# Performance work log

Hardware: AMD Instinct MI355X
Metric: run time of the kernel (lower is better)

Reference implementation:

```python
import jax, jax.numpy as jnp
import numpy as np

FACTOR = 5


def setup_inputs() -> dict:
    key = jax.random.key(0)
    k1, k2, k3, k4 = jax.random.split(key, 4)
    B, L, H, D = 4, 2048, 8, 64
    sample_k = min(FACTOR * int(np.ceil(np.log(L))), L)  # 40
    return {
        "query": jax.random.normal(k1, (B, L, H, D), dtype=jnp.float32),
        "key": jax.random.normal(k2, (B, L, H, D), dtype=jnp.float32),
        "value": jax.random.normal(k3, (B, L, H, D), dtype=jnp.float32),
        "index_sample": jax.random.randint(k4, (L, sample_k), 0, L, dtype=jnp.int32),
    }


def reference(query, key, value, index_sample):
    # query/key/value: (B, L, H, D); mask_flag=True, output_attention=False
    B, L_Q, H, D = query.shape
    L_K = key.shape[1]
    q = jnp.swapaxes(query, 1, 2)  # (B,H,L_Q,D)
    k = jnp.swapaxes(key, 1, 2)    # (B,H,L_K,D)
    v = jnp.swapaxes(value, 1, 2)  # (B,H,L_K,D)

    U_part = min(FACTOR * int(np.ceil(np.log(L_K))), L_K)  # sample_k
    u = min(FACTOR * int(np.ceil(np.log(L_Q))), L_Q)       # n_top

    # --- _prob_QK: sampled QK scores, sparsity measure M, top-u queries ---
    # K_sample: gather sample_k keys per query position -> (B,H,L_Q,sample_k,D)
    K_sample = k[:, :, index_sample, :]
    Q_K_sample = jnp.einsum("bhid,bhisd->bhis", q, K_sample)  # (B,H,L_Q,sample_k)
    M = Q_K_sample.max(axis=-1) - Q_K_sample.sum(axis=-1) / L_K  # (B,H,L_Q)
    _, M_top = jax.lax.top_k(M, u)  # (B,H,u) indices of selected queries

    Q_reduce = jnp.take_along_axis(q, M_top[..., None], axis=2)  # (B,H,u,D)
    scores = jnp.einsum("bhud,bhkd->bhuk", Q_reduce, k)          # (B,H,u,L_K)

    scale = 1.0 / jnp.sqrt(jnp.float32(D))
    scores = scores * scale

    # --- initial context: causal cumsum of V (mask_flag=True) ---
    context = jnp.cumsum(v, axis=2)  # (B,H,L_Q,D)

    # --- update context: causal ProbMask on selected rows, softmax, scatter ---
    # mask[b,h,t,kk] = kk > M_top[b,h,t]
    mask = jnp.arange(L_K)[None, None, None, :] > M_top[..., None]
    scores = jnp.where(mask, -jnp.inf, scores)
    attn = jax.nn.softmax(scores, axis=-1)
    ctx_upd = jnp.einsum("bhuk,bhkd->bhud", attn, v)  # (B,H,u,D)

    b_idx = jnp.arange(context.shape[0])[:, None, None]
    h_idx = jnp.arange(context.shape[1])[None, :, None]
    context = context.at[b_idx, h_idx, M_top].set(ctx_upd)

    return jnp.swapaxes(context, 1, 2)  # (B, L_Q, H, D)
```

## Files before the change

### kernel.cpp

```cpp
#include <hip/hip_runtime.h>
#include <hip/hip_bf16.h>
#include <math.h>

constexpr int B = 4;
constexpr int L = 2048;
constexpr int H = 8;
constexpr int D = 64;
constexpr int S = 40;
constexpr int U = 40;
constexpr int C = 32;
constexpr int CHUNK = L / C;
constexpr int NSEG = 16;
constexpr int SEG  = L / NSEG;
constexpr int PAH  = 688;

__global__ void fused_Mpart(const float* __restrict__ q,
                            const float* __restrict__ k,
                            const float* __restrict__ v,
                            const int*   __restrict__ samp,
                            float* __restrict__ M,
                            float* __restrict__ part) {
    __shared__ float pa[H * PAH];
    int tid = threadIdx.x;

    if (blockIdx.x < 256) {
        int idx = blockIdx.x * 256 + tid;
        int b   = idx >> 14;
        int rem = idx & 16383;
        int c   = rem >> 9;
        int hd  = rem & 511;
        const float* base = v + ((size_t)(b * L + c * CHUNK) * H * D) + hd;
        float s = 0.f;
        for (int i = 0; i < CHUNK; i++) s += base[(size_t)i * (H * D)];
        int h = hd >> 6, d = hd & 63;
        part[((size_t)(b * H + h) * C + c) * D + d] = s;
        return;
    }

    int blk = blockIdx.x - 256;
    int xcd = blk & 7;
    int b   = xcd >> 1;
    int l   = ((blk >> 3) << 1) | (xcd & 1);
    int h      = tid >> 5;
    int lane32 = tid & 31;
    int g  = lane32 >> 4;
    int d4 = lane32 & 15;

    const float4 qv = *(const float4*)(q + ((size_t)(b * L + l) * H + h) * D + d4 * 4);
    const int* srow = samp + l * S;
    float* pah = pa + h * PAH;

#pragma unroll 10
    for (int sb = 0; sb < S; sb += 2) {
        int i0 = srow[sb];
        int i1 = srow[sb + 1];
        int idx = g ? i1 : i0;
        int s = sb + g;
        float4 kv = *(const float4*)(k + ((size_t)(b * L + idx) * H + h) * D + d4 * 4);
        pah[s * 17 + d4] = qv.x * kv.x + qv.y * kv.y + qv.z * kv.z + qv.w * kv.w;
    }
    __syncthreads();

    int s1 = lane32;
    float t0 = 0.f, t1 = 0.f, t2 = 0.f, t3 = 0.f;
#pragma unroll
    for (int i = 0; i < 16; i += 4) {
        t0 += pah[s1 * 17 + i];
        t1 += pah[s1 * 17 + i + 1];
        t2 += pah[s1 * 17 + i + 2];
        t3 += pah[s1 * 17 + i + 3];
    }
    float dot1 = (t0 + t1) + (t2 + t3);
    float mv = dot1, sv = dot1;
    if (lane32 < S - 32) {
        int s2 = 32 + lane32;
        float u0 = 0.f, u1 = 0.f, u2 = 0.f, u3 = 0.f;
#pragma unroll
        for (int i = 0; i < 16; i += 4) {
            u0 += pah[s2 * 17 + i];
            u1 += pah[s2 * 17 + i + 1];
            u2 += pah[s2 * 17 + i + 2];
            u3 += pah[s2 * 17 + i + 3];
        }
        float dot2 = (u0 + u1) + (u2 + u3);
        mv = fmaxf(mv, dot2);
        sv += dot2;
    }
#pragma unroll
    for (int off = 1; off <= 16; off <<= 1) {
        mv = fmaxf(mv, __shfl_xor(mv, off));
        sv += __shfl_xor(sv, off);
    }
    if (lane32 == 0) M[(size_t)(b * H + h) * L + l] = mv - sv * (1.0f / (float)L);
}

__global__ void fused_topk_cumsum(const float* __restrict__ M,
                                  const float* __restrict__ v,
                                  const float* __restrict__ part,
                                  int* __restrict__ Mtop,
                                  float* __restrict__ out) {
    int tid = threadIdx.x;

    if (blockIdx.x >= 32) {
        int idx = (blockIdx.x - 32) * 64 + tid;
        int b   = idx >> 14;
        int rem = idx & 16383;
        int c   = rem >> 9;
        int hd  = rem & 511;
        int h = hd >> 6, d = hd & 63;

        float run = 0.f;
        for (int cc = 0; cc < c; cc++)
            run += part[((size_t)(b * H + h) * C + cc) * D + d];

        const float* base  = v   + ((size_t)(b * L + c * CHUNK) * H * D) + hd;
        float*       obase = out + ((size_t)(b * L + c * CHUNK) * H * D) + hd;
        for (int i = 0; i < CHUNK; i++) {
            run += base[(size_t)i * (H * D)];
            obase[(size_t)i * (H * D)] = run;
        }
        return;
    }

    int bh   = blockIdx.x;
    int base = tid * 32;
    const float* row = M + (size_t)bh * L;

    unsigned int vals[32];
#pragma unroll
    for (int r4 = 0; r4 < 8; r4++) {
        float4 f = *(const float4*)(row + base + r4 * 4);
        const float ff[4] = {f.x, f.y, f.z, f.w};
#pragma unroll
        for (int j = 0; j < 4; j++) {
            unsigned int i = __float_as_uint(ff[j]);
            vals[r4 * 4 + j] = (i & 0x80000000u) ? ~i : (i | 0x80000000u);
        }
    }

    unsigned long long k1 = 0ull, k2 = 0ull;
#pragma unroll
    for (int r = 0; r < 32; r++) {
        unsigned long long kk =
            ((unsigned long long)vals[r] << 32) | (unsigned int)~(base + r);
        if (kk > k1) { k2 = k1; k1 = kk; }
        else if (kk > k2) { k2 = kk; }
    }

    for (int it = 0; it < U; it += 2) {
        unsigned long long a1 = k1, a2 = k2;
#pragma unroll
        for (int off = 1; off < 64; off <<= 1) {
            unsigned long long o1 = __shfl_xor(a1, off);
            unsigned long long o2 = __shfl_xor(a2, off);
            unsigned long long hi = a1 > o1 ? a1 : o1;
            unsigned long long lo = a1 > o1 ? o1 : a1;
            unsigned long long ss = a2 > o2 ? a2 : o2;
            a1 = hi;
            a2 = lo > ss ? lo : ss;
        }
        int i1 = (int)~(unsigned int)a1;
        int i2 = (int)~(unsigned int)a2;
        if (tid == 0) {
            Mtop[bh * U + it]     = i1;
            Mtop[bh * U + it + 1] = i2;
        }
        bool own1 = (i1 >> 5) == tid;
        bool own2 = (i2 >> 5) == tid;
        if (own1 | own2) {
            int r1 = own1 ? (i1 & 31) : 32;
            int r2 = own2 ? (i2 & 31) : 32;
#pragma unroll
            for (int r = 0; r < 32; r++)
                if (r == r1 || r == r2) vals[r] = 0u;
            k1 = 0ull; k2 = 0ull;
#pragma unroll
            for (int r = 0; r < 32; r++) {
                unsigned long long kk =
                    ((unsigned long long)vals[r] << 32) | (unsigned int)~(base + r);
                if (kk > k1) { k2 = k1; k1 = kk; }
                else if (kk > k2) { k2 = kk; }
            }
        }
    }
}

__global__ __launch_bounds__(256, 2)
void attn_batched(const float* __restrict__ q,
                  const float* __restrict__ k,
                  const float* __restrict__ v,
                  const int*   __restrict__ Mtop,
                  float* __restrict__ ml,
                  float* __restrict__ pacc) {
    int blk = blockIdx.x;
    int xcd = blk & 7;
    int b   = xcd >> 1;
    int r   = ((blk >> 3) << 1) | (xcd & 1);
    int h   = r >> 4;
    int seg = r & 15;
    int bh  = b * H + h;
    int j0  = seg * SEG;
    int tid = threadIdx.x;

    __shared__ float Qs[U * D];
    __shared__ float KV[SEG * D];
    __shared__ float Sc[U * SEG];
    __shared__ float red[U * 4];
    __shared__ float mrow[U];
    __shared__ int   qis[U];

    if (tid < U) qis[tid] = Mtop[bh * U + tid];
    __syncthreads();

    for (int i = tid; i < U * 16; i += 256) {
        int u = i >> 4, d4 = i & 15;
        *(float4*)&Qs[u * D + d4 * 4] =
            *(const float4*)(q + ((size_t)(b * L + qis[u]) * H + h) * D + d4 * 4);
    }
    for (int i = tid; i < SEG * 16; i += 256) {
        int rr = i >> 4, d4 = i & 15;
        float4 kv = *(const float4*)(k + ((size_t)(b * L + j0 + rr) * H + h) * D + d4 * 4);
        *(float4*)&KV[rr * D + (d4 ^ (rr & 15)) * 4] = kv;
    }
    __syncthreads();

    int ug = tid >> 5;
    int jg = tid & 31;
    int jlow = jg & 15;
    float acc[5][4];
#pragma unroll
    for (int uu = 0; uu < 5; uu++)
#pragma unroll
        for (int jj = 0; jj < 4; jj++) acc[uu][jj] = 0.f;

#pragma unroll
    for (int kk4 = 0; kk4 < 16; kk4++) {
        float4 kf[4];
        int slot = kk4 ^ jlow;
#pragma unroll
        for (int jj = 0; jj < 4; jj++)
            kf[jj] = *(const float4*)&KV[(jg + 32 * jj) * D + slot * 4];
#pragma unroll
        for (int uu = 0; uu < 5; uu++) {
            float4 qf = *(const float4*)&Qs[(ug * 5 + uu) * D + kk4 * 4];
#pragma unroll
            for (int jj = 0; jj < 4; jj++) {
                acc[uu][jj] += qf.x * kf[jj].x + qf.y * kf[jj].y
                             + qf.z * kf[jj].z + qf.w * kf[jj].w;
            }
        }
    }
#pragma unroll
    for (int uu = 0; uu < 5; uu++) {
        int u = ug * 5 + uu;
        int um = u & 15;
#pragma unroll
        for (int jj = 0; jj < 4; jj++) {
            int j = jg + 32 * jj;
            Sc[u * SEG + 4 * ((j >> 2) ^ um) + (j & 3)] = acc[uu][jj] * 0.125f;
        }
    }
    __syncthreads();

    for (int i = tid; i < SEG * 16; i += 256) {
        int rr = i >> 4, d4 = i & 15;
        float4 vv = *(const float4*)(v + ((size_t)(b * L + j0 + rr) * H + h) * D + d4 * 4);
        *(float4*)&KV[rr * D + (d4 ^ (rr & 15)) * 4] = vv;
    }

    int su = tid >> 2, sq = tid & 3;
    int nkc = 0;
    if (tid < U * 4) {
        int nk = qis[su] + 1 - j0;
        nkc = nk < 0 ? 0 : (nk > SEG ? SEG : nk);
        int um = su & 15;
        float mvx = -INFINITY;
        for (int t = 0; t < 32; t++) {
            int i = sq + 4 * t;
            if (i < nkc) mvx = fmaxf(mvx, Sc[su * SEG + 4 * ((i >> 2) ^ um) + (i & 3)]);
        }
        red[su * 4 + sq] = mvx;
    }
    __syncthreads();
    if (tid < U) {
        float m = fmaxf(fmaxf(red[tid * 4], red[tid * 4 + 1]),
                        fmaxf(red[tid * 4 + 2], red[tid * 4 + 3]));
        mrow[tid] = m;
    }
    __syncthreads();
    if (tid < U * 4) {
        float m = mrow[su];
        int um = su & 15;
        float ls = 0.f;
        for (int t = 0; t < 32; t++) {
            int i = sq + 4 * t;
            int addr = su * SEG + 4 * ((i >> 2) ^ um) + (i & 3);
            float e = 0.f;
            if (i < nkc) e = __expf(Sc[addr] - m);
            Sc[addr] = e;
            ls += e;
        }
        red[su * 4 + sq] = ls;
    }
    __syncthreads();
    if (tid < U) {
        float ls = (red[tid * 4] + red[tid * 4 + 1]) + (red[tid * 4 + 2] + red[tid * 4 + 3]);
        size_t mli = 2 * ((size_t)(bh * U + tid) * NSEG + seg);
        ml[mli]     = mrow[tid];
        ml[mli + 1] = ls;
    }

    int vg = jg;
    float a2[5][2];
#pragma unroll
    for (int uu = 0; uu < 5; uu++) { a2[uu][0] = 0.f; a2[uu][1] = 0.f; }

    for (int j4 = 0; j4 < 32; j4++) {
        float4 pf[5];
#pragma unroll
        for (int uu = 0; uu < 5; uu++) {
            int u = ug * 5 + uu;
            pf[uu] = *(const float4*)&Sc[u * SEG + 4 * (j4 ^ (u & 15))];
        }
#pragma unroll
        for (int jj = 0; jj < 4; jj++) {
            int j = j4 * 4 + jj;
            int fo = 4 * ((vg >> 1) ^ (j & 15)) + ((2 * vg) & 3);
            float2 vv = *(const float2*)&KV[j * D + fo];
#pragma unroll
            for (int uu = 0; uu < 5; uu++) {
                float p = ((const float*)&pf[uu])[jj];
                a2[uu][0] += p * vv.x;
                a2[uu][1] += p * vv.y;
            }
        }
    }
#pragma unroll
    for (int uu = 0; uu < 5; uu++) {
        int u = ug * 5 + uu;
        float2 w2 = make_float2(a2[uu][0], a2[uu][1]);
        *(float2*)&pacc[((size_t)(bh * U + u) * NSEG + seg) * D + 2 * vg] = w2;
    }
}

__global__ void attn_combine(const int* __restrict__ Mtop,
                             const float* __restrict__ ml,
                             const float* __restrict__ pacc,
                             float* __restrict__ out) {
    int blk = blockIdx.x;
    int u  = blk % U;
    int bh = blk / U;
    int h  = bh % H;
    int b  = bh / H;
    int d  = threadIdx.x;
    int qi = Mtop[bh * U + u];

    size_t r0 = (size_t)blk * NSEG;
    float m = -INFINITY;
#pragma unroll
    for (int s = 0; s < NSEG; s++) m = fmaxf(m, ml[2 * (r0 + s)]);

    float lt = 0.f, acc = 0.f;
#pragma unroll
    for (int s = 0; s < NSEG; s++) {
        float ms = ml[2 * (r0 + s)];
        float w  = __expf(ms - m);
        lt  += ml[2 * (r0 + s) + 1] * w;
        acc += pacc[(r0 + s) * D + d] * w;
    }
    out[((size_t)(b * L + qi) * H + h) * D + d] = acc / lt;
}

extern "C" void kernel_launch(void* const* d_in, const int* in_sizes, int n_in,
                              void* d_out, int out_size, void* d_ws, size_t ws_size,
                              hipStream_t stream) {
    const float* q    = (const float*)d_in[0];
    const float* k    = (const float*)d_in[1];
    const float* v    = (const float*)d_in[2];
    const int*   samp = (const int*)d_in[3];
    float* out = (float*)d_out;

    float* M    = (float*)d_ws;
    int*   Mtop = (int*)(M + (size_t)B * H * L);
    float* part = (float*)(Mtop + (size_t)B * H * U);
    float* ml   = part + (size_t)B * H * C * D;
    float* pacc = ml + (size_t)B * H * U * NSEG * 2;

    fused_Mpart<<<256 + B * L, 256, 0, stream>>>(q, k, v, samp, M, part);
    fused_topk_cumsum<<<32 + 1024, 64, 0, stream>>>(M, v, part, Mtop, out);
    attn_batched<<<B * H * NSEG, 256, 0, stream>>>(q, k, v, Mtop, ml, pacc);
    attn_combine<<<B * H * U, 64, 0, stream>>>(Mtop, ml, pacc, out);
}
```

Measured before the change: 184.2 us.

## Fuse softmax into score registers with shuffles; vectorize PV; widen cumsum blocks

```diff
diff --git a/kernel.cpp b/kernel.cpp
--- a/kernel.cpp
+++ b/kernel.cpp
@@ -102,7 +102,7 @@
     int tid = threadIdx.x;
 
     if (blockIdx.x >= 32) {
-        int idx = (blockIdx.x - 32) * 64 + tid;
+        int idx = (blockIdx.x - 32) * 256 + tid;
         int b   = idx >> 14;
         int rem = idx & 16383;
         int c   = rem >> 9;
@@ -122,6 +122,7 @@
         return;
     }
 
+    if (tid >= 64) return;
     int bh   = blockIdx.x;
     int base = tid * 32;
     const float* row = M + (size_t)bh * L;
@@ -205,8 +206,6 @@
     __shared__ float Qs[U * D];
     __shared__ float KV[SEG * D];
     __shared__ float Sc[U * SEG];
-    __shared__ float red[U * 4];
-    __shared__ float mrow[U];
     __shared__ int   qis[U];
 
     if (tid < U) qis[tid] = Mtop[bh * U + tid];
@@ -250,14 +249,39 @@
             }
         }
     }
+
 #pragma unroll
     for (int uu = 0; uu < 5; uu++) {
-        int u = ug * 5 + uu;
+        int u  = ug * 5 + uu;
         int um = u & 15;
+        int nk = qis[u] + 1 - j0;
+        nk = nk < 0 ? 0 : (nk > SEG ? SEG : nk);
+        float sc4[4];
+        float mv = -INFINITY;
 #pragma unroll
         for (int jj = 0; jj < 4; jj++) {
             int j = jg + 32 * jj;
-            Sc[u * SEG + 4 * ((j >> 2) ^ um) + (j & 3)] = acc[uu][jj] * 0.125f;
+            sc4[jj] = acc[uu][jj] * 0.125f;
+            if (j < nk) mv = fmaxf(mv, sc4[jj]);
+        }
+#pragma unroll
+        for (int off = 1; off <= 16; off <<= 1)
+            mv = fmaxf(mv, __shfl_xor(mv, off));
+        float ls = 0.f;
+#pragma unroll
+        for (int jj = 0; jj < 4; jj++) {
+            int j = jg + 32 * jj;
+            float e = (j < nk) ? __expf(sc4[jj] - mv) : 0.f;
+            Sc[u * SEG + 4 * ((j >> 2) ^ um) + (j & 3)] = e;
+            ls += e;
+        }
+#pragma unroll
+        for (int off = 1; off <= 16; off <<= 1)
+            ls += __shfl_xor(ls, off);
+        if (jg == 0) {
+            size_t mli = 2 * ((size_t)(bh * U + u) * NSEG + seg);
+            ml[mli]     = mv;
+            ml[mli + 1] = ls;
         }
     }
     __syncthreads();
@@ -267,55 +291,18 @@
         float4 vv = *(const float4*)(v + ((size_t)(b * L + j0 + rr) * H + h) * D + d4 * 4);
         *(float4*)&KV[rr * D + (d4 ^ (rr & 15)) * 4] = vv;
     }
-
-    int su = tid >> 2, sq = tid & 3;
-    int nkc = 0;
-    if (tid < U * 4) {
-        int nk = qis[su] + 1 - j0;
-        nkc = nk < 0 ? 0 : (nk > SEG ? SEG : nk);
-        int um = su & 15;
-        float mvx = -INFINITY;
-        for (int t = 0; t < 32; t++) {
-            int i = sq + 4 * t;
-            if (i < nkc) mvx = fmaxf(mvx, Sc[su * SEG + 4 * ((i >> 2) ^ um) + (i & 3)]);
-        }
-        red[su * 4 + sq] = mvx;
-    }
-    __syncthreads();
-    if (tid < U) {
-        float m = fmaxf(fmaxf(red[tid * 4], red[tid * 4 + 1]),
-                        fmaxf(red[tid * 4 + 2], red[tid * 4 + 3]));
-        mrow[tid] = m;
-    }
-    __syncthreads();
-    if (tid < U * 4) {
-        float m = mrow[su];
-        int um = su & 15;
-        float ls = 0.f;
-        for (int t = 0; t < 32; t++) {
-            int i = sq + 4 * t;
-            int addr = su * SEG + 4 * ((i >> 2) ^ um) + (i & 3);
-            float e = 0.f;
-            if (i < nkc) e = __expf(Sc[addr] - m);
-            Sc[addr] = e;
-            ls += e;
-        }
-        red[su * 4 + sq] = ls;
-    }
-    __syncthreads();
-    if (tid < U) {
-        float ls = (red[tid * 4] + red[tid * 4 + 1]) + (red[tid * 4 + 2] + red[tid * 4 + 3]);
-        size_t mli = 2 * ((size_t)(bh * U + tid) * NSEG + seg);
-        ml[mli]     = mrow[tid];
-        ml[mli + 1] = ls;
-    }
-
-    int vg = jg;
-    float a2[5][2];
-#pragma unroll
-    for (int uu = 0; uu < 5; uu++) { a2[uu][0] = 0.f; a2[uu][1] = 0.f; }
-
-    for (int j4 = 0; j4 < 32; j4++) {
+    __syncthreads();
+
+    int r5 = tid & 31;
+    int dg = r5 >> 1;
+    int jh = r5 & 1;
+    float4 a4[5];
+#pragma unroll
+    for (int uu = 0; uu < 5; uu++) a4[uu] = make_float4(0.f, 0.f, 0.f, 0.f);
+
+#pragma unroll 4
+    for (int jq = 0; jq < 16; jq++) {
+        int j4 = jh * 16 + jq;
         float4 pf[5];
 #pragma unroll
         for (int uu = 0; uu < 5; uu++) {
@@ -325,21 +312,31 @@
 #pragma unroll
         for (int jj = 0; jj < 4; jj++) {
             int j = j4 * 4 + jj;
-            int fo = 4 * ((vg >> 1) ^ (j & 15)) + ((2 * vg) & 3);
-            float2 vv = *(const float2*)&KV[j * D + fo];
+            float4 vv = *(const float4*)&KV[j * D + (dg ^ (j & 15)) * 4];
 #pragma unroll
             for (int uu = 0; uu < 5; uu++) {
                 float p = ((const float*)&pf[uu])[jj];
-                a2[uu][0] += p * vv.x;
-                a2[uu][1] += p * vv.y;
+                a4[uu].x += p * vv.x;
+                a4[uu].y += p * vv.y;
+                a4[uu].z += p * vv.z;
+                a4[uu].w += p * vv.w;
             }
         }
     }
-#pragma unroll
-    for (int uu = 0; uu < 5; uu++) {
-        int u = ug * 5 + uu;
-        float2 w2 = make_float2(a2[uu][0], a2[uu][1]);
-        *(float2*)&pacc[((size_t)(bh * U + u) * NSEG + seg) * D + 2 * vg] = w2;
+    if (jh == 1) {
+#pragma unroll
+        for (int uu = 0; uu < 5; uu++)
+            *(float4*)&Qs[(ug * 5 + uu) * D + dg * 4] = a4[uu];
+    }
+    __syncthreads();
+    if (jh == 0) {
+#pragma unroll
+        for (int uu = 0; uu < 5; uu++) {
+            int u = ug * 5 + uu;
+            float4 o = *(const float4*)&Qs[u * D + dg * 4];
+            o.x += a4[uu].x; o.y += a4[uu].y; o.z += a4[uu].z; o.w += a4[uu].w;
+            *(float4*)&pacc[((size_t)(bh * U + u) * NSEG + seg) * D + dg * 4] = o;
+        }
     }
 }
 
@@ -387,7 +384,7 @@
     float* pacc = ml + (size_t)B * H * U * NSEG * 2;
 
     fused_Mpart<<<256 + B * L, 256, 0, stream>>>(q, k, v, samp, M, part);
-    fused_topk_cumsum<<<32 + 1024, 64, 0, stream>>>(M, v, part, Mtop, out);
+    fused_topk_cumsum<<<32 + 256, 256, 0, stream>>>(M, v, part, Mtop, out);
     attn_batched<<<B * H * NSEG, 256, 0, stream>>>(q, k, v, Mtop, ml, pacc);
     attn_combine<<<B * H * U, 64, 0, stream>>>(Mtop, ml, pacc, out);
 }
```

Result: slower. 316.6 us (+71.9%).
